# Kernel optimization log

Measured on AMD Instinct MI355X. Metric: run time of the kernel, lower is better.

The kernel has to match this reference:

```python
import jax, jax.numpy as jnp
import numpy as np

B, S, E, H = 2, 2048, 1024, 16
DH = E // H  # 64


def setup_inputs() -> dict:
    key = jax.random.key(0)
    ks = jax.random.split(key, 9)
    sc = 1.0 / np.sqrt(E)
    return {
        "x": jax.random.normal(ks[0], (B, S, E), dtype=jnp.float32),
        "Wq": jax.random.normal(ks[1], (E, E), dtype=jnp.float32) * sc,
        "bq": jax.random.normal(ks[2], (E,), dtype=jnp.float32) * 0.02,
        "Wk": jax.random.normal(ks[3], (E, E), dtype=jnp.float32) * sc,
        "bk": jax.random.normal(ks[4], (E,), dtype=jnp.float32) * 0.02,
        "Wv": jax.random.normal(ks[5], (E, E), dtype=jnp.float32) * sc,
        "bv": jax.random.normal(ks[6], (E,), dtype=jnp.float32) * 0.02,
        "Wo": jax.random.normal(ks[7], (E, E), dtype=jnp.float32) * sc,
        "bo": jax.random.normal(ks[8], (E,), dtype=jnp.float32) * 0.02,
    }


def reference(x, Wq, bq, Wk, bk, Wv, bv, Wo, bo):
    b, s, e = x.shape
    h, dh = H, e // H
    # NOTE: original torch code does .view(B, H, S, Dh) on the [B, S, E]
    # projection WITHOUT transposing first; we replicate that exact reshape.
    q = (x @ Wq.T + bq).reshape(b, h, s, dh)
    k = (x @ Wk.T + bk).reshape(b, h, s, dh)
    v = (x @ Wv.T + bv).reshape(b, h, s, dh)
    scale = 1.0 / jnp.sqrt(jnp.asarray(dh, dtype=x.dtype))
    scores = jax.nn.softmax(jnp.einsum("bhqd,bhkd->bhqk", q, k) * scale, axis=-1)
    out = jnp.einsum("bhqk,bhkd->bhqd", scores, v)  # [B,H,S,Dh]
    out = out.transpose(0, 2, 1, 3).reshape(b, s, e)  # matches torch transpose(1,2).view
    return out @ Wo.T + bo
```

## Files before the change

### kernel.cpp

```cpp
#include <hip/hip_runtime.h>
#include <hip/hip_bf16.h>
#include <stdint.h>

typedef __bf16 bf16x8 __attribute__((ext_vector_type(8)));
typedef float  f32x4  __attribute__((ext_vector_type(4)));
typedef float  f32x16 __attribute__((ext_vector_type(16)));
typedef __hip_bfloat16 bf16;

__device__ __forceinline__ void gll16(const void* g, void* l) {
    typedef const unsigned int __attribute__((address_space(1)))* gp_t;
    typedef unsigned int __attribute__((address_space(3)))* lp_t;
    __builtin_amdgcn_global_load_lds((gp_t)(g), (lp_t)(l), 16, 0, 0);
}

__device__ __forceinline__ float fexp2(float x) {
#if __has_builtin(__builtin_amdgcn_exp2f)
    return __builtin_amdgcn_exp2f(x);
#else
    float r; asm volatile("v_exp_f32 %0, %1" : "=v"(r) : "v"(x)); return r;
#endif
}

__device__ __forceinline__ float tsum16(const f32x16& v) {
    float a0 = v[0] + v[1],   a1 = v[2] + v[3];
    float a2 = v[4] + v[5],   a3 = v[6] + v[7];
    float a4 = v[8] + v[9],   a5 = v[10] + v[11];
    float a6 = v[12] + v[13], a7 = v[14] + v[15];
    float b0 = a0 + a1, b1 = a2 + a3, b2 = a4 + a5, b3 = a6 + a7;
    return (b0 + b1) + (b2 + b3);
}

__global__ __launch_bounds__(256) void prep_convert(
    const float* __restrict__ x,
    const float* __restrict__ wq, const float* __restrict__ wk,
    const float* __restrict__ wv, const float* __restrict__ wo,
    bf16* __restrict__ Xb, bf16* __restrict__ Wcat, bf16* __restrict__ Wob)
{
    int i = blockIdx.x * blockDim.x + threadIdx.x;
    int base = i * 4;
    const float* src; bf16* dst;
    if      (base < 4194304) { src = x  + base;             dst = Xb   + base; }
    else if (base < 5242880) { src = wq + (base - 4194304); dst = Wcat + (base - 4194304); }
    else if (base < 6291456) { src = wk + (base - 5242880); dst = Wcat + 1048576 + (base - 5242880); }
    else if (base < 7340032) { src = wv + (base - 6291456); dst = Wcat + 2097152 + (base - 6291456); }
    else                     { src = wo + (base - 7340032); dst = Wob  + (base - 7340032); }
    float4 v = *(const float4*)src;
    union { bf16 h[4]; ushort4 u; } cv;
    cv.h[0] = __float2bfloat16(v.x);
    cv.h[1] = __float2bfloat16(v.y);
    cv.h[2] = __float2bfloat16(v.z);
    cv.h[3] = __float2bfloat16(v.w);
    *(ushort4*)dst = cv.u;
}

__global__ __launch_bounds__(256, 2) void gemm_qkv(
    const bf16* __restrict__ X, const bf16* __restrict__ Wc,
    const float* __restrict__ bq, const float* __restrict__ bk, const float* __restrict__ bv,
    bf16* __restrict__ Pq, bf16* __restrict__ Pk, bf16* __restrict__ Pv)
{
    __shared__ __align__(16) bf16 Ab[128 * 32];
    __shared__ __align__(16) bf16 Bb[128 * 32];
    const int id = blockIdx.x;
    const int sid = (id & 7) * 96 + (id >> 3);
    const int t = threadIdx.x;
    const int lane = t & 63, w = t >> 6;
    const int lr = lane & 15, lg = lane >> 4;
    const int wr = w >> 1, wc = w & 1;
    const int row0 = (sid / 24) * 128, col0 = (sid % 24) * 128;

    f32x4 acc[4][4] = {};

    const char* Xc  = (const char*)X;
    const char* Wcc = (const char*)Wc;
    char* AbC = (char*)Ab;
    char* BbC = (char*)Bb;
    const int o0 = t * 16, o1 = o0 + 4096;
    const int ldsoff = w * 1024;

    for (int k0 = 0; k0 < 1024; k0 += 32) {
        __syncthreads();
        gll16(Xc  + (size_t)(row0 + (o0 >> 6)) * 2048 + (size_t)k0 * 2 + (o0 & 63), AbC + ldsoff);
        gll16(Wcc + (size_t)(col0 + (o0 >> 6)) * 2048 + (size_t)k0 * 2 + (o0 & 63), BbC + ldsoff);
        gll16(Xc  + (size_t)(row0 + (o1 >> 6)) * 2048 + (size_t)k0 * 2 + (o1 & 63), AbC + 4096 + ldsoff);
        gll16(Wcc + (size_t)(col0 + (o1 >> 6)) * 2048 + (size_t)k0 * 2 + (o1 & 63), BbC + 4096 + ldsoff);
        __syncthreads();
        bf16x8 af[4], bw[4];
        #pragma unroll
        for (int i = 0; i < 4; ++i)
            af[i] = *(const bf16x8*)(AbC + ((wr * 64 + i * 16 + lr) * 32 + lg * 8) * 2);
        #pragma unroll
        for (int j = 0; j < 4; ++j)
            bw[j] = *(const bf16x8*)(BbC + ((wc * 64 + j * 16 + lr) * 32 + lg * 8) * 2);
        #pragma unroll
        for (int i = 0; i < 4; ++i)
            #pragma unroll
            for (int j = 0; j < 4; ++j)
                acc[i][j] = __builtin_amdgcn_mfma_f32_16x16x32_bf16(af[i], bw[j], acc[i][j], 0, 0, 0);
    }

    const int mid = col0 >> 10;
    const float* bias = (mid == 0) ? bq : (mid == 1 ? bk : bv);
    bf16* Out = (mid == 0) ? Pq : (mid == 1 ? Pk : Pv);
    const float scale = (mid == 0) ? 0.125f * 1.44269504f : 1.0f;
    const int nc0 = col0 - (mid << 10) + wc * 64;
    const int mr0 = row0 + wr * 64;
    #pragma unroll
    for (int i = 0; i < 4; ++i)
        #pragma unroll
        for (int j = 0; j < 4; ++j) {
            int cc = nc0 + j * 16 + lr;
            float bsv = bias[cc];
            #pragma unroll
            for (int p = 0; p < 4; ++p) {
                int rr = mr0 + i * 16 + lg * 4 + p;
                Out[(size_t)rr * 1024 + cc] = __float2bfloat16((acc[i][j][p] + bsv) * scale);
            }
        }
}

__global__ __launch_bounds__(256) void transpose_v(const bf16* __restrict__ Pv, bf16* __restrict__ Vt)
{
    __shared__ bf16 tile[64][72];
    const int head = blockIdx.y;
    const int st   = blockIdx.x;
    const bf16* src = Pv + (size_t)head * 131072 + (size_t)st * 4096;
    bf16* dst = Vt + (size_t)head * 131072 + (size_t)st * 64;
    const int t = threadIdx.x;
    const int rr = t >> 2, c0 = (t & 3) * 16;
    #pragma unroll
    for (int u = 0; u < 2; ++u) {
        bf16x8 v = *(const bf16x8*)(src + rr * 64 + c0 + u * 8);
        #pragma unroll
        for (int e = 0; e < 8; ++e) tile[rr][c0 + u * 8 + e] = ((const bf16*)&v)[e];
    }
    __syncthreads();
    #pragma unroll
    for (int u = 0; u < 2; ++u) {
        bf16 ov[8];
        #pragma unroll
        for (int e = 0; e < 8; ++e) {
            int y = u * 8 + e;
            int z = (y & 3) | ((y & 8) >> 1) | ((y & 4) << 1);
            ov[e] = tile[c0 + z][rr];
        }
        *(bf16x8*)(dst + (size_t)rr * 2048 + c0 + u * 8) = *(const bf16x8*)ov;
    }
}

__global__ __launch_bounds__(512, 4) void attn_fwd(
    const bf16* __restrict__ Pq, const bf16* __restrict__ Pk,
    const bf16* __restrict__ Vt, bf16* __restrict__ Of)
{
    __shared__ __align__(16) bf16 Kl[2][128 * 64];
    __shared__ __align__(16) bf16 Vl[2][64 * 128];

    const int blk0 = blockIdx.x;
    const int blk = (blk0 & 7) * 64 + (blk0 >> 3);
    const int head = blk >> 4;
    const int qt = blk & 15;
    const int bb = head >> 4, hh = head & 15;
    const bf16* Qh = Pq + (size_t)head * 131072;
    const char* Khc = (const char*)(Pk + (size_t)head * 131072);
    const char* Vhc = (const char*)(Vt + (size_t)head * 131072);

    const int t = threadIdx.x;
    const int lane = t & 63, w = t >> 6;
    const int qg = w & 3, kh = w >> 2;
    const int ql = lane & 31, hi = lane >> 5;
    const int q0 = qt * 128 + qg * 32;

    bf16x8 qf[4];
    #pragma unroll
    for (int m = 0; m < 4; ++m)
        qf[m] = *(const bf16x8*)(Qh + (size_t)(q0 + ql) * 64 + m * 16 + hi * 8);

    f32x16 acc[2] = {};
    float l_run = 0.f;

    const int stg_key = t >> 3, stg_ks = t & 7;
    const int stg_d   = t >> 4, stg_vs = t & 15;
    const size_t kgo = (size_t)stg_key * 128 + ((stg_ks ^ (stg_key & 7)) * 16);
    const size_t vgo = (size_t)stg_d * 4096 + ((stg_vs ^ (stg_d & 15)) * 16);
    const int ldst = w * 1024;

#define STAGE(S0, BUF)                                                          \
    {                                                                           \
        char* KB = (char*)(Kl[BUF]);                                            \
        char* VB = (char*)(Vl[BUF]);                                            \
        _Pragma("unroll")                                                       \
        for (int qq = 0; qq < 2; ++qq) {                                        \
            gll16(Khc + (size_t)(S0) * 128 + (size_t)qq * 8192 + kgo,           \
                  KB + qq * 8192 + ldst);                                       \
            gll16(Vhc + (size_t)(S0) * 2 + (size_t)qq * 131072 + vgo,           \
                  VB + qq * 8192 + ldst);                                       \
        }                                                                       \
    }

    STAGE(0, 0);
    STAGE(128, 1);

    int cur = 0;
    for (int s0 = 0; s0 < 2048; s0 += 128) {
        if (s0 < 1920) {
            asm volatile("s_waitcnt vmcnt(4)\n\ts_barrier" ::: "memory");
        } else {
            asm volatile("s_waitcnt vmcnt(0)\n\ts_barrier" ::: "memory");
        }

        const char* KlC = (const char*)(Kl[cur]);
        const char* VlC = (const char*)(Vl[cur]);

        f32x16 sa[2] = {};
        __builtin_amdgcn_s_setprio(1);
        #pragma unroll
        for (int kb = 0; kb < 2; ++kb) {
            int row = kh * 64 + kb * 32 + ql;
            #pragma unroll
            for (int m = 0; m < 4; ++m) {
                int byt = row * 128 + ((32 * m + 16 * hi) ^ ((row & 7) << 4));
                bf16x8 kf = *(const bf16x8*)(KlC + byt);
                sa[kb] = __builtin_amdgcn_mfma_f32_32x32x16_bf16(kf, qf[m], sa[kb], 0, 0, 0);
            }
        }
        __builtin_amdgcn_s_setprio(0);

        #pragma unroll
        for (int kb = 0; kb < 2; ++kb)
            #pragma unroll
            for (int r = 0; r < 16; ++r)
                sa[kb][r] = fexp2(sa[kb][r]);
        l_run += tsum16(sa[0]) + tsum16(sa[1]);

        __builtin_amdgcn_s_setprio(1);
        #pragma unroll
        for (int sbl = 0; sbl < 4; ++sbl) {
            const int kb = sbl >> 1, par = (sbl & 1) * 8;
            const int sbg = kh * 4 + sbl;
            bf16x8 pa;
            #pragma unroll
            for (int e = 0; e < 8; ++e) pa[e] = (__bf16)sa[kb][par + e];
            #pragma unroll
            for (int db = 0; db < 2; ++db) {
                int row = db * 32 + ql;
                int byt = row * 256 + ((sbg * 32 + hi * 16) ^ ((row & 15) << 4));
                bf16x8 vf = *(const bf16x8*)(VlC + byt);
                acc[db] = __builtin_amdgcn_mfma_f32_32x32x16_bf16(vf, pa, acc[db], 0, 0, 0);
            }
        }
        __builtin_amdgcn_s_setprio(0);

        __builtin_amdgcn_s_barrier();
        if (s0 + 256 < 2048) STAGE(s0 + 256, cur);
        cur ^= 1;
    }
#undef STAGE

    l_run += __shfl_xor(l_run, 32);

    float* cb1 = (float*)Kl;
    float* cb2 = (float*)Vl;
    const int idx = qg * 64 + lane;
    if (kh == 1) {
        #pragma unroll
        for (int r = 0; r < 16; ++r) cb1[idx * 17 + r] = acc[0][r];
        cb1[idx * 17 + 16] = l_run;
        #pragma unroll
        for (int r = 0; r < 16; ++r) cb2[idx * 17 + r] = acc[1][r];
    }
    __syncthreads();
    if (kh == 0) {
        float inv = 1.0f / (l_run + cb1[idx * 17 + 16]);
        bf16* orow = Of + (size_t)(bb * 2048 + q0 + ql) * 1024 + hh * 64;
        #pragma unroll
        for (int db = 0; db < 2; ++db)
            #pragma unroll
            for (int g = 0; g < 4; ++g) {
                union { bf16 h[4]; ushort4 u; } ob;
                #pragma unroll
                for (int j = 0; j < 4; ++j) {
                    int r = 4 * g + j;
                    float p1 = (db == 0) ? cb1[idx * 17 + r] : cb2[idx * 17 + r];
                    ob.h[j] = __float2bfloat16((acc[db][r] + p1) * inv);
                }
                *(ushort4*)(orow + db * 32 + 8 * g + 4 * hi) = ob.u;
            }
    }
}

__global__ __launch_bounds__(256, 2) void gemm_out(
    const bf16* __restrict__ A, const bf16* __restrict__ W,
    const float* __restrict__ bo, float* __restrict__ C)
{
    __shared__ __align__(16) bf16 Ab[64 * 32];
    __shared__ __align__(16) bf16 Bb[128 * 32];
    const int id = blockIdx.x;
    const int sid = (id & 7) * 64 + (id >> 3);
    const int t = threadIdx.x;
    const int lane = t & 63, w = t >> 6;
    const int lr = lane & 15, lg = lane >> 4;
    const int wr = w >> 1, wc = w & 1;
    const int row0 = (sid >> 3) * 64, col0 = (sid & 7) * 128;

    f32x4 acc[2][4] = {};
    const char* Ac = (const char*)A;
    const char* Wc = (const char*)W;
    char* AbC = (char*)Ab;
    char* BbC = (char*)Bb;
    const int o0 = t * 16, o1 = o0 + 4096;
    const int ldsoff = w * 1024;

    for (int k0 = 0; k0 < 1024; k0 += 32) {
        __syncthreads();
        gll16(Ac + (size_t)(row0 + (o0 >> 6)) * 2048 + (size_t)k0 * 2 + (o0 & 63), AbC + ldsoff);
        gll16(Wc + (size_t)(col0 + (o0 >> 6)) * 2048 + (size_t)k0 * 2 + (o0 & 63), BbC + ldsoff);
        gll16(Wc + (size_t)(col0 + (o1 >> 6)) * 2048 + (size_t)k0 * 2 + (o1 & 63), BbC + 4096 + ldsoff);
        __syncthreads();
        bf16x8 af[2], bw[4];
        #pragma unroll
        for (int i = 0; i < 2; ++i)
            af[i] = *(const bf16x8*)(AbC + ((wr * 32 + i * 16 + lr) * 32 + lg * 8) * 2);
        #pragma unroll
        for (int j = 0; j < 4; ++j)
            bw[j] = *(const bf16x8*)(BbC + ((wc * 64 + j * 16 + lr) * 32 + lg * 8) * 2);
        #pragma unroll
        for (int i = 0; i < 2; ++i)
            #pragma unroll
            for (int j = 0; j < 4; ++j)
                acc[i][j] = __builtin_amdgcn_mfma_f32_16x16x32_bf16(af[i], bw[j], acc[i][j], 0, 0, 0);
    }

    const int nc0 = col0 + wc * 64;
    const int mr0 = row0 + wr * 32;
    #pragma unroll
    for (int i = 0; i < 2; ++i)
        #pragma unroll
        for (int j = 0; j < 4; ++j) {
            int cc = nc0 + j * 16 + lr;
            float bsv = bo[cc];
            #pragma unroll
            for (int p = 0; p < 4; ++p) {
                int rr = mr0 + i * 16 + lg * 4 + p;
                C[(size_t)rr * 1024 + cc] = acc[i][j][p] + bsv;
            }
        }
}

extern "C" void kernel_launch(void* const* d_in, const int* in_sizes, int n_in,
                              void* d_out, int out_size, void* d_ws, size_t ws_size,
                              hipStream_t stream) {
    const float* x  = (const float*)d_in[0];
    const float* Wq = (const float*)d_in[1];
    const float* bq = (const float*)d_in[2];
    const float* Wk = (const float*)d_in[3];
    const float* bk = (const float*)d_in[4];
    const float* Wv = (const float*)d_in[5];
    const float* bv = (const float*)d_in[6];
    const float* Wo = (const float*)d_in[7];
    const float* bo = (const float*)d_in[8];
    float* out = (float*)d_out;

    char* ws = (char*)d_ws;
    bf16* Xb   = (bf16*)(ws + 0);
    bf16* Wcat = (bf16*)(ws + 8388608);
    bf16* Wob  = (bf16*)(ws + 14680064);
    bf16* Pq   = (bf16*)(ws + 16777216);
    bf16* Pk   = (bf16*)(ws + 25165824);
    bf16* Pv   = (bf16*)(ws + 33554432);
    bf16* Vt   = (bf16*)(ws + 0);
    bf16* Of   = (bf16*)(ws + 33554432);
    (void)ws_size; (void)in_sizes; (void)n_in; (void)out_size;

    prep_convert<<<8192, 256, 0, stream>>>(x, Wq, Wk, Wv, Wo, Xb, Wcat, Wob);
    gemm_qkv<<<768, 256, 0, stream>>>(Xb, Wcat, bq, bk, bv, Pq, Pk, Pv);
    transpose_v<<<dim3(32, 32), 256, 0, stream>>>(Pv, Vt);
    attn_fwd<<<512, 512, 0, stream>>>(Pq, Pk, Vt, Of);
    gemm_out<<<512, 256, 0, stream>>>(Of, Wob, bo, out);
}
```

Before: 112.1 us.

## Double-buffer LDS tiles in QKV and output GEMMs with async prefetch

Both projection GEMMs now use two LDS buffers and issue the global-to-LDS loads for step k+64 while computing on the current tile. Manual s_waitcnt vmcnt counts let the next stage's loads stay in flight across the barrier. The aim is to hide global load latency behind MFMA work. The cost is doubled LDS use, which may limit occupancy, and correctness now depends on the hand-written vmcnt values and on whether LDS reads have completed before the post-compute barrier.

```diff
diff --git a/kernel.cpp b/kernel.cpp
--- a/kernel.cpp
+++ b/kernel.cpp
@@ -58,8 +58,8 @@
     const float* __restrict__ bq, const float* __restrict__ bk, const float* __restrict__ bv,
     bf16* __restrict__ Pq, bf16* __restrict__ Pk, bf16* __restrict__ Pv)
 {
-    __shared__ __align__(16) bf16 Ab[128 * 32];
-    __shared__ __align__(16) bf16 Bb[128 * 32];
+    __shared__ __align__(16) bf16 Ab[2][128 * 32];
+    __shared__ __align__(16) bf16 Bb[2][128 * 32];
     const int id = blockIdx.x;
     const int sid = (id & 7) * 96 + (id >> 3);
     const int t = threadIdx.x;
@@ -72,18 +72,34 @@
 
     const char* Xc  = (const char*)X;
     const char* Wcc = (const char*)Wc;
-    char* AbC = (char*)Ab;
-    char* BbC = (char*)Bb;
     const int o0 = t * 16, o1 = o0 + 4096;
     const int ldsoff = w * 1024;
 
+#define GSTAGE(K0, BUF)                                                               \
+    {                                                                                 \
+        char* AB = (char*)(Ab[BUF]);                                                  \
+        char* BB = (char*)(Bb[BUF]);                                                  \
+        gll16(Xc  + (size_t)(row0 + (o0 >> 6)) * 2048 + (size_t)(K0) * 2 + (o0 & 63), \
+              AB + ldsoff);                                                           \
+        gll16(Wcc + (size_t)(col0 + (o0 >> 6)) * 2048 + (size_t)(K0) * 2 + (o0 & 63), \
+              BB + ldsoff);                                                           \
+        gll16(Xc  + (size_t)(row0 + (o1 >> 6)) * 2048 + (size_t)(K0) * 2 + (o1 & 63), \
+              AB + 4096 + ldsoff);                                                    \
+        gll16(Wcc + (size_t)(col0 + (o1 >> 6)) * 2048 + (size_t)(K0) * 2 + (o1 & 63), \
+              BB + 4096 + ldsoff);                                                    \
+    }
+
+    GSTAGE(0, 0);
+    GSTAGE(32, 1);
+    int cur = 0;
     for (int k0 = 0; k0 < 1024; k0 += 32) {
-        __syncthreads();
-        gll16(Xc  + (size_t)(row0 + (o0 >> 6)) * 2048 + (size_t)k0 * 2 + (o0 & 63), AbC + ldsoff);
-        gll16(Wcc + (size_t)(col0 + (o0 >> 6)) * 2048 + (size_t)k0 * 2 + (o0 & 63), BbC + ldsoff);
-        gll16(Xc  + (size_t)(row0 + (o1 >> 6)) * 2048 + (size_t)k0 * 2 + (o1 & 63), AbC + 4096 + ldsoff);
-        gll16(Wcc + (size_t)(col0 + (o1 >> 6)) * 2048 + (size_t)k0 * 2 + (o1 & 63), BbC + 4096 + ldsoff);
-        __syncthreads();
+        if (k0 < 992) {
+            asm volatile("s_waitcnt vmcnt(4)\n\ts_barrier" ::: "memory");
+        } else {
+            asm volatile("s_waitcnt vmcnt(0)\n\ts_barrier" ::: "memory");
+        }
+        const char* AbC = (const char*)(Ab[cur]);
+        const char* BbC = (const char*)(Bb[cur]);
         bf16x8 af[4], bw[4];
         #pragma unroll
         for (int i = 0; i < 4; ++i)
@@ -96,7 +112,11 @@
             #pragma unroll
             for (int j = 0; j < 4; ++j)
                 acc[i][j] = __builtin_amdgcn_mfma_f32_16x16x32_bf16(af[i], bw[j], acc[i][j], 0, 0, 0);
-    }
+        __builtin_amdgcn_s_barrier();
+        if (k0 + 64 < 1024) GSTAGE(k0 + 64, cur);
+        cur ^= 1;
+    }
+#undef GSTAGE
 
     const int mid = col0 >> 10;
     const float* bias = (mid == 0) ? bq : (mid == 1 ? bk : bv);
@@ -291,8 +311,8 @@
     const bf16* __restrict__ A, const bf16* __restrict__ W,
     const float* __restrict__ bo, float* __restrict__ C)
 {
-    __shared__ __align__(16) bf16 Ab[64 * 32];
-    __shared__ __align__(16) bf16 Bb[128 * 32];
+    __shared__ __align__(16) bf16 Ab[2][64 * 32];
+    __shared__ __align__(16) bf16 Bb[2][128 * 32];
     const int id = blockIdx.x;
     const int sid = (id & 7) * 64 + (id >> 3);
     const int t = threadIdx.x;
@@ -304,17 +324,32 @@
     f32x4 acc[2][4] = {};
     const char* Ac = (const char*)A;
     const char* Wc = (const char*)W;
-    char* AbC = (char*)Ab;
-    char* BbC = (char*)Bb;
     const int o0 = t * 16, o1 = o0 + 4096;
     const int ldsoff = w * 1024;
 
+#define OSTAGE(K0, BUF)                                                               \
+    {                                                                                 \
+        char* AB = (char*)(Ab[BUF]);                                                  \
+        char* BB = (char*)(Bb[BUF]);                                                  \
+        gll16(Ac + (size_t)(row0 + (o0 >> 6)) * 2048 + (size_t)(K0) * 2 + (o0 & 63),  \
+              AB + ldsoff);                                                           \
+        gll16(Wc + (size_t)(col0 + (o0 >> 6)) * 2048 + (size_t)(K0) * 2 + (o0 & 63),  \
+              BB + ldsoff);                                                           \
+        gll16(Wc + (size_t)(col0 + (o1 >> 6)) * 2048 + (size_t)(K0) * 2 + (o1 & 63),  \
+              BB + 4096 + ldsoff);                                                    \
+    }
+
+    OSTAGE(0, 0);
+    OSTAGE(32, 1);
+    int cur = 0;
     for (int k0 = 0; k0 < 1024; k0 += 32) {
-        __syncthreads();
-        gll16(Ac + (size_t)(row0 + (o0 >> 6)) * 2048 + (size_t)k0 * 2 + (o0 & 63), AbC + ldsoff);
-        gll16(Wc + (size_t)(col0 + (o0 >> 6)) * 2048 + (size_t)k0 * 2 + (o0 & 63), BbC + ldsoff);
-        gll16(Wc + (size_t)(col0 + (o1 >> 6)) * 2048 + (size_t)k0 * 2 + (o1 & 63), BbC + 4096 + ldsoff);
-        __syncthreads();
+        if (k0 < 992) {
+            asm volatile("s_waitcnt vmcnt(3)\n\ts_barrier" ::: "memory");
+        } else {
+            asm volatile("s_waitcnt vmcnt(0)\n\ts_barrier" ::: "memory");
+        }
+        const char* AbC = (const char*)(Ab[cur]);
+        const char* BbC = (const char*)(Bb[cur]);
         bf16x8 af[2], bw[4];
         #pragma unroll
         for (int i = 0; i < 2; ++i)
@@ -327,7 +362,11 @@
             #pragma unroll
             for (int j = 0; j < 4; ++j)
                 acc[i][j] = __builtin_amdgcn_mfma_f32_16x16x32_bf16(af[i], bw[j], acc[i][j], 0, 0, 0);
-    }
+        __builtin_amdgcn_s_barrier();
+        if (k0 + 64 < 1024) OSTAGE(k0 + 64, cur);
+        cur ^= 1;
+    }
+#undef OSTAGE
 
     const int nc0 = col0 + wc * 64;
     const int mr0 = row0 + wr * 32;
```

After: 111.3 us, median of 2. About the same (-0.8%).
